# Optimization experiments

Measured on AMD Instinct MI355X. Metric: run time of the kernel, lower is better.

Reference implementation:

```python
import jax, jax.numpy as jnp
import numpy as np

B, S, H, Z = 32, 2048, 256, 64
TEMPERATURE = float(H) ** 0.5
NEG_INF = -1e9


def setup_inputs() -> dict:
    key = jax.random.key(0)
    ks = jax.random.split(key, 8)
    return {
        "encoder_hidden_states": jax.random.normal(ks[0], (B, S, H), dtype=jnp.float32),
        "decoder_hidden_states": jax.random.normal(ks[1], (B, S, H), dtype=jnp.float32),
        "decoder_final_hidden_state": jax.random.normal(ks[2], (B, H), dtype=jnp.float32),
        "latent_z_seq": jax.random.normal(ks[3], (B, S, Z), dtype=jnp.float32),
        "mask": jax.random.randint(ks[4], (B, S), 0, 2).astype(bool),
        "Wq": jax.random.normal(ks[5], (H, H), dtype=jnp.float32),
        "Wk": jax.random.normal(ks[6], (H, H), dtype=jnp.float32),
        "Wv": jax.random.normal(ks[7], (Z, Z), dtype=jnp.float32),
    }


def reference(encoder_hidden_states, decoder_hidden_states, decoder_final_hidden_state,
              latent_z_seq, mask, Wq, Wk, Wv):
    # Projections
    k = jnp.einsum('bsh,hd->bsd', encoder_hidden_states, Wk)
    q = jnp.einsum('bsh,hd->bsd', decoder_hidden_states, Wq)
    v = jnp.einsum('bsz,zd->bsd', latent_z_seq, Wv)
    # alignment[b, i, j] = q_i . k_j / sqrt(H)   -> [B, S, S]
    alignment = jnp.einsum('bid,bjd->bij', q, k) / TEMPERATURE
    # mask over QUERY positions (axis -2), broadcast along key axis (-1)
    alignment = jnp.where(mask[:, :, None], alignment, NEG_INF)
    # NOTE: non-standard softmax over the query axis (dim=-2)
    attn = jax.nn.softmax(alignment, axis=-2)
    output = jnp.einsum('bij,bjd->bid', attn, v)  # [B, S, Z]
    return output, attn
```

## Files before the change

kernel.cpp:

```cpp
#include <hip/hip_runtime.h>
#include <stdint.h>

#define B_  32
#define S_  2048
#define H_  256
#define Z_  64

typedef unsigned short u16;
typedef __attribute__((ext_vector_type(8))) short bf16x8;
typedef __attribute__((ext_vector_type(4))) float f32x4;

__device__ __forceinline__ u16 f2bf(float f) {
    unsigned int x = __float_as_uint(f);
    x = (x + 0x7fffu + ((x >> 16) & 1u)) >> 16;
    return (u16)x;
}
__device__ __forceinline__ float bf2f(u16 u) {
    return __uint_as_float(((unsigned int)u) << 16);
}

__device__ __forceinline__ void gl2lds16(const void* g, void* l) {
    __builtin_amdgcn_global_load_lds(
        (const __attribute__((address_space(1))) unsigned int*)g,
        (__attribute__((address_space(3))) unsigned int*)l,
        16, 0, 0);
}

__global__ void detect_kernel(const u16* __restrict__ wq, int* __restrict__ flag) {
    __shared__ int tot;
    const int t = threadIdx.x;
    if (t == 0) tot = 0;
    __syncthreads();
    int cnt = 0;
    #pragma unroll
    for (int r = 0; r < 16; ++r) {
        u16 u = wq[(r * 256 + t) * 2];
        int e = (u >> 7) & 0xFF;
        cnt += (u == 0 || (e >= 107 && e <= 132)) ? 1 : 0;
    }
    atomicAdd(&tot, cnt);
    __syncthreads();
    if (t == 0) *flag = (tot < 2048) ? 1 : 0;
}

__device__ void role_mask(int bx, const void* __restrict__ raw, int* __restrict__ mi) {
    __shared__ int isByte;
    const int t = threadIdx.x;
    if (t == 0) isByte = 0;
    __syncthreads();
    const unsigned int* w = (const unsigned int*)raw;
    if (w[t & 255] > 1u) isByte = 1;
    __syncthreads();
    int e = bx * 256 + t;
    int val;
    if (isByte) val = ((const unsigned char*)raw)[e] ? 1 : 0;
    else        val = w[e] ? 1 : 0;
    mi[e] = val;
}

__device__ void role_wsplit(int bx, int by, int fp32,
                            const void* __restrict__ Wq, const void* __restrict__ Wk,
                            u16* __restrict__ WqTh, u16* __restrict__ WqTl,
                            u16* __restrict__ WkTh, u16* __restrict__ WkTl) {
    const void* src = by ? Wk : Wq;
    u16* oh = by ? WkTh : WqTh;
    u16* ol = by ? WkTl : WqTl;
    int base = bx * 1024;
    #pragma unroll
    for (int r = 0; r < 4; ++r) {
        int idx = base + r * 256 + threadIdx.x;
        int d = idx >> 8, h = idx & 255;
        float v = fp32 ? ((const float*)src)[h * 256 + d]
                       : bf2f(((const u16*)src)[h * 256 + d]);
        u16 hi = f2bf(v);
        oh[idx] = hi;
        ol[idx] = f2bf(v - bf2f(hi));
    }
}

__device__ void role_xsplit(int bx, int by, int fp32,
                            const void* __restrict__ dec, const void* __restrict__ enc,
                            u16* __restrict__ Xdh, u16* __restrict__ Xdl,
                            u16* __restrict__ Xeh, u16* __restrict__ Xel) {
    const void* src = by ? enc : dec;
    u16* oh = by ? Xeh : Xdh;
    u16* ol = by ? Xel : Xdl;
    const int t = threadIdx.x;
    const size_t blockbase = (size_t)bx * 4096;
    if (fp32) {
        const float4* s4 = (const float4*)src;
        #pragma unroll
        for (int j = 0; j < 4; ++j) {
            size_t idx = blockbase + j * 1024 + t * 4;
            float4 v = s4[idx >> 2];
            u16 h0 = f2bf(v.x), h1 = f2bf(v.y), h2 = f2bf(v.z), h3 = f2bf(v.w);
            u16 l0 = f2bf(v.x - bf2f(h0)), l1 = f2bf(v.y - bf2f(h1));
            u16 l2 = f2bf(v.z - bf2f(h2)), l3 = f2bf(v.w - bf2f(h3));
            uint2 ph, pl;
            ph.x = (unsigned)h0 | ((unsigned)h1 << 16);
            ph.y = (unsigned)h2 | ((unsigned)h3 << 16);
            pl.x = (unsigned)l0 | ((unsigned)l1 << 16);
            pl.y = (unsigned)l2 | ((unsigned)l3 << 16);
            ((uint2*)oh)[idx >> 2] = ph;
            ((uint2*)ol)[idx >> 2] = pl;
        }
    } else {
        const uint2* s2 = (const uint2*)src;
        #pragma unroll
        for (int j = 0; j < 4; ++j) {
            size_t idx = blockbase + j * 1024 + t * 4;
            uint2 r = s2[idx >> 2];
            uint2 z; z.x = 0u; z.y = 0u;
            ((uint2*)oh)[idx >> 2] = r;
            ((uint2*)ol)[idx >> 2] = z;
        }
    }
}

__device__ void role_vproj(int bx, int dc, int fp32,
                           const void* __restrict__ Lraw,
                           const void* __restrict__ Wvraw, u16* __restrict__ vT) {
    __shared__ float wv[64 * 16];
    const int t = threadIdx.x;
    #pragma unroll
    for (int r = 0; r < 4; ++r) {
        int idx = r * 256 + t;
        int z = idx >> 4, dd = idx & 15;
        wv[idx] = fp32 ? ((const float*)Wvraw)[z * 64 + dc * 16 + dd]
                       : bf2f(((const u16*)Wvraw)[z * 64 + dc * 16 + dd]);
    }
    __syncthreads();
    const int flat = bx * 256 + t;
    const int b = flat >> 11, s = flat & 2047;

    float lz[64];
    if (fp32) {
        const float4* lr = (const float4*)((const float*)Lraw + (size_t)flat * 64);
        #pragma unroll
        for (int c = 0; c < 16; ++c) {
            float4 v = lr[c];
            lz[c * 4 + 0] = v.x; lz[c * 4 + 1] = v.y;
            lz[c * 4 + 2] = v.z; lz[c * 4 + 3] = v.w;
        }
    } else {
        const uint4* lr = (const uint4*)((const u16*)Lraw + (size_t)flat * 64);
        #pragma unroll
        for (int c = 0; c < 8; ++c) {
            uint4 v = lr[c];
            unsigned wd[4] = {v.x, v.y, v.z, v.w};
            #pragma unroll
            for (int e2 = 0; e2 < 4; ++e2) {
                lz[c * 8 + e2 * 2 + 0] = bf2f((u16)(wd[e2] & 0xffffu));
                lz[c * 8 + e2 * 2 + 1] = bf2f((u16)(wd[e2] >> 16));
            }
        }
    }

    float acc[16];
    #pragma unroll
    for (int d = 0; d < 16; ++d) acc[d] = 0.f;
    for (int z = 0; z < 64; ++z) {
        float lv = lz[z];
        const float4* wrow = (const float4*)&wv[z * 16];
        #pragma unroll
        for (int d4 = 0; d4 < 4; ++d4) {
            float4 wq = wrow[d4];
            acc[d4 * 4 + 0] += lv * wq.x;
            acc[d4 * 4 + 1] += lv * wq.y;
            acc[d4 * 4 + 2] += lv * wq.z;
            acc[d4 * 4 + 3] += lv * wq.w;
        }
    }
    #pragma unroll
    for (int d = 0; d < 16; ++d)
        vT[((size_t)b * 64 + dc * 16 + d) * S_ + s] = f2bf(acc[d]);
}

__global__ __launch_bounds__(256) void prep_kernel(
        const int* __restrict__ flagp, int n_xs,
        const void* __restrict__ dec, const void* __restrict__ enc,
        u16* __restrict__ Xdh, u16* __restrict__ Xdl,
        u16* __restrict__ Xeh, u16* __restrict__ Xel,
        const void* __restrict__ Lraw, const void* __restrict__ Wvraw,
        u16* __restrict__ vT,
        const void* __restrict__ Wq, const void* __restrict__ Wk,
        u16* __restrict__ WqTh, u16* __restrict__ WqTl,
        u16* __restrict__ WkTh, u16* __restrict__ WkTl,
        const void* __restrict__ mraw, int* __restrict__ maskI)
{
    const int fp32 = *flagp;
    int r = blockIdx.x;
    if (r < n_xs) {
        role_xsplit(r & 4095, r >> 12, fp32, dec, enc, Xdh, Xdl, Xeh, Xel);
        return;
    }
    r -= n_xs;
    if (r < 1024) {
        role_vproj(r & 255, r >> 8, fp32, Lraw, Wvraw, vT);
        return;
    }
    r -= 1024;
    if (r < 128) {
        role_wsplit(r & 63, r >> 6, fp32, Wq, Wk, WqTh, WqTl, WkTh, WkTl);
        return;
    }
    r -= 128;
    role_mask(r, mraw, maskI);
}

__global__ __launch_bounds__(256, 2) void proj_kernel(
        const int* __restrict__ flagp, int use_xsplit,
        const float* __restrict__ Xf0, const u16* __restrict__ Xu0,
        const u16* __restrict__ Xh0, const u16* __restrict__ Xl0,
        const u16* __restrict__ WTh0, const u16* __restrict__ WTl0,
        u16* __restrict__ Ph0, u16* __restrict__ Pl0,
        const float* __restrict__ Xf1, const u16* __restrict__ Xu1,
        const u16* __restrict__ Xh1, const u16* __restrict__ Xl1,
        const u16* __restrict__ WTh1, const u16* __restrict__ WTl1,
        u16* __restrict__ Ph1, u16* __restrict__ Pl1)
{
    __shared__ __align__(16) u16 lds[16384];
    const int z = blockIdx.z;
    const float* Xf = z ? Xf1 : Xf0;
    const u16*   Xu = z ? Xu1 : Xu0;
    const u16*   Xh = z ? Xh1 : Xh0;
    const u16*   Xl = z ? Xl1 : Xl0;
    const u16*  WTh = z ? WTh1 : WTh0;
    const u16*  WTl = z ? WTl1 : WTl0;
    u16* Ph = z ? Ph1 : Ph0;
    u16* Pl = z ? Pl1 : Pl0;

    const int fp32 = *flagp;
    const int t = threadIdx.x;
    const int lane = t & 63, w = t >> 6;
    const int i0 = blockIdx.x * 128;
    const int d0 = blockIdx.y * 128;
    const int rh = w >> 1, ch = w & 1;
    const int l15 = lane & 15;
    const int c0 = lane >> 4;

    const int srow = t >> 3;
    const int scp  = t & 7;
    const int sc   = scp ^ (srow & 7);
    const int scol = (sc & 3) * 8;
    const int slo  = sc & 4;

    f32x4 acc[4][4];
    #pragma unroll
    for (int a = 0; a < 4; ++a)
        #pragma unroll
        for (int c = 0; c < 4; ++c) acc[a][c] = (f32x4){0.f, 0.f, 0.f, 0.f};

    for (int ks = 0; ks < 8; ++ks) {
        const int kc = ks * 32;
        {
            const u16* wsrc = slo ? WTl : WTh;
            #pragma unroll
            for (int rep = 0; rep < 4; ++rep) {
                int s = t + rep * 256;
                int row = srow + rep * 32;
                gl2lds16(wsrc + (size_t)(d0 + row) * H_ + kc + scol, lds + 8192 + s * 8);
            }
        }
        if (use_xsplit) {
            const u16* xsrc = slo ? Xl : Xh;
            #pragma unroll
            for (int rep = 0; rep < 4; ++rep) {
                int s = t + rep * 256;
                int row = srow + rep * 32;
                gl2lds16(xsrc + (size_t)(i0 + row) * H_ + kc + scol, lds + s * 8);
            }
        } else if (fp32) {
            #pragma unroll
            for (int rep = 0; rep < 2; ++rep) {
                int s = t + rep * 256;
                int r = s >> 2, c8 = s & 3;
                const float4* src = (const float4*)(Xf + (size_t)(i0 + r) * H_ + kc + c8 * 8);
                float4 x0 = src[0], x1 = src[1];
                float xs[8] = {x0.x, x0.y, x0.z, x0.w, x1.x, x1.y, x1.z, x1.w};
                unsigned hh[8], ll[8];
                #pragma unroll
                for (int j = 0; j < 8; ++j) {
                    u16 hb = f2bf(xs[j]);
                    hh[j] = hb;
                    ll[j] = f2bf(xs[j] - bf2f(hb));
                }
                uint4 ph, pl;
                ph.x = hh[0] | (hh[1] << 16); ph.y = hh[2] | (hh[3] << 16);
                ph.z = hh[4] | (hh[5] << 16); ph.w = hh[6] | (hh[7] << 16);
                pl.x = ll[0] | (ll[1] << 16); pl.y = ll[2] | (ll[3] << 16);
                pl.z = ll[4] | (ll[5] << 16); pl.w = ll[6] | (ll[7] << 16);
                int posH = c8 ^ (r & 7);
                *(uint4*)(lds + r * 64 + posH * 8) = ph;
                *(uint4*)(lds + r * 64 + (posH ^ 4) * 8) = pl;
            }
        } else {
            #pragma unroll
            for (int rep = 0; rep < 2; ++rep) {
                int s = t + rep * 256;
                int r = s >> 2, c8 = s & 3;
                uint4 raw = *(const uint4*)(Xu + (size_t)(i0 + r) * H_ + kc + c8 * 8);
                int posH = c8 ^ (r & 7);
                *(uint4*)(lds + r * 64 + posH * 8) = raw;
                *(uint4*)(lds + r * 64 + (posH ^ 4) * 8) = (uint4){0u, 0u, 0u, 0u};
            }
        }
        __syncthreads();
        bf16x8 ah[4], al[4], bh[4], bl[4];
        #pragma unroll
        for (int f = 0; f < 4; ++f) {
            int ra = rh * 64 + f * 16 + l15;
            int rb = ch * 64 + f * 16 + l15;
            int pa = c0 ^ (ra & 7);
            int pb = c0 ^ (rb & 7);
            ah[f] = *(const bf16x8*)(lds + ra * 64 + pa * 8);
            al[f] = *(const bf16x8*)(lds + ra * 64 + (pa ^ 4) * 8);
            bh[f] = *(const bf16x8*)(lds + 8192 + rb * 64 + pb * 8);
            bl[f] = *(const bf16x8*)(lds + 8192 + rb * 64 + (pb ^ 4) * 8);
        }
        #pragma unroll
        for (int fr = 0; fr < 4; ++fr)
            #pragma unroll
            for (int fc = 0; fc < 4; ++fc) {
                acc[fr][fc] = __builtin_amdgcn_mfma_f32_16x16x32_bf16(al[fr], bh[fc], acc[fr][fc], 0, 0, 0);
                acc[fr][fc] = __builtin_amdgcn_mfma_f32_16x16x32_bf16(ah[fr], bl[fc], acc[fr][fc], 0, 0, 0);
                acc[fr][fc] = __builtin_amdgcn_mfma_f32_16x16x32_bf16(ah[fr], bh[fc], acc[fr][fc], 0, 0, 0);
            }
        __syncthreads();
    }
    #pragma unroll
    for (int fr = 0; fr < 4; ++fr)
        #pragma unroll
        for (int fc = 0; fc < 4; ++fc)
            #pragma unroll
            for (int reg = 0; reg < 4; ++reg) {
                float v = acc[fr][fc][reg];
                int i = i0 + rh * 64 + fr * 16 + (lane >> 4) * 4 + reg;
                int d = d0 + ch * 64 + fc * 16 + l15;
                u16 hi = f2bf(v);
                u16 lo = f2bf(v - bf2f(hi));
                size_t off = (size_t)i * H_ + d;
                Ph[off] = hi;
                Pl[off] = lo;
            }
}

__global__ __launch_bounds__(256, 2) void qk_kernel(
        const u16* __restrict__ qh, const u16* __restrict__ ql,
        const u16* __restrict__ kh, const u16* __restrict__ kl,
        const int* __restrict__ maskI, u16* __restrict__ attnB,
        float* __restrict__ attnF, u16* __restrict__ stageB, int use_stage,
        float* __restrict__ m_p, float* __restrict__ s_p,
        int b0, const int* __restrict__ flagp)
{
    __shared__ __align__(16) char smem[35328];
    u16*  stage = (u16*)smem;
    u16*  etile = (u16*)smem;
    float* cmax = (float*)(smem + 32768);
    float* csum = (float*)(smem + 33792);
    float* mrow = (float*)(smem + 34816);

    const int fp32 = *flagp;
    const int t = threadIdx.x;
    const int lane = t & 63, w = t >> 6;
    const int jt = blockIdx.x, it = blockIdx.y, bz = blockIdx.z;
    const int b = b0 + bz;
    const int i0 = it * 128, j0 = jt * 128;
    const int rh = w >> 1, ch = w & 1;
    const int l15 = lane & 15;
    const int c0 = lane >> 4;

    if (t < 128) mrow[t] = (maskI[b * S_ + i0 + t] != 0) ? 1.f : 0.f;

    const size_t qbase = ((size_t)bz * S_ + i0) * H_;
    const size_t kbase = ((size_t)bz * S_ + j0) * H_;

    const int srow = t >> 3;
    const int scp  = t & 7;
    const int sc   = scp ^ (srow & 7);
    const int scol = (sc & 3) * 8;
    const u16* qsrc = (sc & 4) ? ql : qh;
    const u16* ksrc = (sc & 4) ? kl : kh;

    f32x4 acc[4][4];
    #pragma unroll
    for (int a = 0; a < 4; ++a)
        #pragma unroll
        for (int c = 0; c < 4; ++c) acc[a][c] = (f32x4){0.f, 0.f, 0.f, 0.f};

    for (int ks = 0; ks < 8; ++ks) {
        const int kc = ks * 32;
        #pragma unroll
        for (int rep = 0; rep < 4; ++rep) {
            int s = t + rep * 256;
            int row = srow + rep * 32;
            gl2lds16(qsrc + qbase + (size_t)row * H_ + kc + scol, stage + s * 8);
            gl2lds16(ksrc + kbase + (size_t)row * H_ + kc + scol, stage + 8192 + s * 8);
        }
        __syncthreads();
        bf16x8 ah[4], al[4], bh[4], bl[4];
        #pragma unroll
        for (int f = 0; f < 4; ++f) {
            int ra = rh * 64 + f * 16 + l15;
            int rb = ch * 64 + f * 16 + l15;
            int pa = c0 ^ (ra & 7);
            int pb = c0 ^ (rb & 7);
            ah[f] = *(const bf16x8*)(stage + ra * 64 + pa * 8);
            al[f] = *(const bf16x8*)(stage + ra * 64 + (pa ^ 4) * 8);
            bh[f] = *(const bf16x8*)(stage + 8192 + rb * 64 + pb * 8);
            bl[f] = *(const bf16x8*)(stage + 8192 + rb * 64 + (pb ^ 4) * 8);
        }
        #pragma unroll
        for (int fr = 0; fr < 4; ++fr)
            #pragma unroll
            for (int fc = 0; fc < 4; ++fc) {
                acc[fr][fc] = __builtin_amdgcn_mfma_f32_16x16x32_bf16(al[fr], bh[fc], acc[fr][fc], 0, 0, 0);
                acc[fr][fc] = __builtin_amdgcn_mfma_f32_16x16x32_bf16(ah[fr], bl[fc], acc[fr][fc], 0, 0, 0);
                acc[fr][fc] = __builtin_amdgcn_mfma_f32_16x16x32_bf16(ah[fr], bh[fc], acc[fr][fc], 0, 0, 0);
            }
        __syncthreads();
    }

    const float inv_t = 0.0625f;
    float mloc[4] = {-3e38f, -3e38f, -3e38f, -3e38f};
    #pragma unroll
    for (int fr = 0; fr < 4; ++fr)
        #pragma unroll
        for (int reg = 0; reg < 4; ++reg) {
            float keep = mrow[rh * 64 + fr * 16 + (lane >> 4) * 4 + reg];
            #pragma unroll
            for (int fc = 0; fc < 4; ++fc) {
                float l = acc[fr][fc][reg] * inv_t;
                l = (keep != 0.f) ? l : -1e9f;
                acc[fr][fc][reg] = l;
                mloc[fc] = fmaxf(mloc[fc], l);
            }
        }
    #pragma unroll
    for (int fc = 0; fc < 4; ++fc) {
        mloc[fc] = fmaxf(mloc[fc], __shfl_xor(mloc[fc], 16, 64));
        mloc[fc] = fmaxf(mloc[fc], __shfl_xor(mloc[fc], 32, 64));
    }
    if (lane < 16) {
        #pragma unroll
        for (int fc = 0; fc < 4; ++fc)
            cmax[rh * 128 + ch * 64 + fc * 16 + lane] = mloc[fc];
    }
    __syncthreads();

    float mcol[4], sloc[4];
    #pragma unroll
    for (int fc = 0; fc < 4; ++fc) {
        int c = ch * 64 + fc * 16 + l15;
        mcol[fc] = fmaxf(cmax[c], cmax[128 + c]);
        sloc[fc] = 0.f;
    }
    #pragma unroll
    for (int fr = 0; fr < 4; ++fr)
        #pragma unroll
        for (int reg = 0; reg < 4; ++reg) {
            int row = rh * 64 + fr * 16 + (lane >> 4) * 4 + reg;
            #pragma unroll
            for (int fc = 0; fc < 4; ++fc) {
                float e = __expf(acc[fr][fc][reg] - mcol[fc]);
                sloc[fc] += e;
                etile[row * 128 + ch * 64 + fc * 16 + l15] = f2bf(e);
            }
        }
    #pragma unroll
    for (int fc = 0; fc < 4; ++fc) {
        sloc[fc] += __shfl_xor(sloc[fc], 16, 64);
        sloc[fc] += __shfl_xor(sloc[fc], 32, 64);
    }
    if (lane < 16) {
        #pragma unroll
        for (int fc = 0; fc < 4; ++fc)
            csum[rh * 128 + ch * 64 + fc * 16 + lane] = sloc[fc];
    }
    __syncthreads();

    if (t < 128) {
        float m = fmaxf(cmax[t], cmax[128 + t]);
        float sres = csum[t] + csum[128 + t];
        size_t so = ((size_t)b * 16 + it) * S_ + j0 + t;
        m_p[so] = m;
        s_p[so] = sres;
    }
    const size_t abase = ((size_t)b * S_ + i0) * S_ + j0;
    if (fp32) {
        if (use_stage) {
            #pragma unroll
            for (int rep = 0; rep < 8; ++rep) {
                int s = t + rep * 256;
                int row = s >> 4, off = (s & 15) * 8;
                *(uint4*)(stageB + abase + (size_t)row * S_ + off) = *(const uint4*)(etile + s * 8);
            }
        } else {
            #pragma unroll
            for (int rep = 0; rep < 8; ++rep) {
                int s = t + rep * 256;
                int row = s >> 4, off = (s & 15) * 8;
                const u16* src = etile + s * 8;
                float* gp = attnF + abase + (size_t)row * S_ + off;
                float4 f0, f1;
                f0.x = bf2f(src[0]); f0.y = bf2f(src[1]); f0.z = bf2f(src[2]); f0.w = bf2f(src[3]);
                f1.x = bf2f(src[4]); f1.y = bf2f(src[5]); f1.z = bf2f(src[6]); f1.w = bf2f(src[7]);
                *(float4*)gp = f0;
                *(float4*)(gp + 4) = f1;
            }
        }
    } else {
        #pragma unroll
        for (int rep = 0; rep < 8; ++rep) {
            int s = t + rep * 256;
            int row = s >> 4, off = (s & 15) * 8;
            *(uint4*)(attnB + abase + (size_t)row * S_ + off) = *(const uint4*)(etile + s * 8);
        }
    }
}

__global__ __launch_bounds__(256) void stats_kernel(
        const float* __restrict__ m_p, const float* __restrict__ s_p, float* __restrict__ scl)
{
    int id = blockIdx.x * 256 + threadIdx.x;
    int b = id >> 11, j = id & 2047;
    float mv[16];
    float M = -3e38f;
    #pragma unroll
    for (int itile = 0; itile < 16; ++itile) {
        mv[itile] = m_p[((size_t)b * 16 + itile) * S_ + j];
        M = fmaxf(M, mv[itile]);
    }
    float L = 0.f;
    #pragma unroll
    for (int itile = 0; itile < 16; ++itile)
        L += s_p[((size_t)b * 16 + itile) * S_ + j] * __expf(mv[itile] - M);
    float invL = (L > 0.f) ? (1.f / L) : 0.f;
    #pragma unroll
    for (int itile = 0; itile < 16; ++itile)
        scl[((size_t)b * 16 + itile) * S_ + j] = __expf(mv[itile] - M) * invL;
}

__global__ __launch_bounds__(256, 2) void av_gemm_kernel(
        const u16* __restrict__ vT, const float* __restrict__ scl,
        const u16* __restrict__ stageB, u16* __restrict__ attnB,
        float* __restrict__ attnF,
        u16* __restrict__ outB, float* __restrict__ outF,
        const int* __restrict__ flagp)
{
    __shared__ __align__(16) u16 lds_attn[128 * 128];
    __shared__ __align__(16) u16 lds_vt[64 * 128];
    const int fp32 = *flagp;
    const u16* srcE = fp32 ? stageB : attnB;
    const int t = threadIdx.x;
    const int lane = t & 63, w = t >> 6;
    const int it = blockIdx.x, b = blockIdx.y;
    const int i0 = it * 128;
    const int l15 = lane & 15;

    const int acp = t & 15;
    const int arow0 = t >> 4;
    const int ac = acp ^ (arow0 & 15);
    const int vpos = (t & 15) ^ (t >> 4);
    const int j8 = (t & 15) * 8;

    f32x4 acc[2][4];
    #pragma unroll
    for (int a = 0; a < 2; ++a)
        #pragma unroll
        for (int c = 0; c < 4; ++c) acc[a][c] = (f32x4){0.f, 0.f, 0.f, 0.f};

    for (int jt = 0; jt < 16; ++jt) {
        const int j0 = jt * 128;
        __syncthreads();
        const size_t abase = ((size_t)b * S_ + i0) * S_ + j0;
        #pragma unroll
        for (int rep = 0; rep < 8; ++rep) {
            int s = t + rep * 256;
            int row = arow0 + rep * 16;
            gl2lds16(srcE + abase + (size_t)row * S_ + ac * 8, lds_attn + s * 8);
        }
        float sc[8], esc[8];
        {
            const float4* sp = (const float4*)(scl + ((size_t)b * 16 + it) * S_ + j0 + j8);
            float4 s0 = sp[0], s1 = sp[1];
            sc[0] = s0.x; sc[1] = s0.y; sc[2] = s0.z; sc[3] = s0.w;
            sc[4] = s1.x; sc[5] = s1.y; sc[6] = s1.z; sc[7] = s1.w;
            const float4* ep = (const float4*)(scl + ((size_t)b * 16 + it) * S_ + j0 + ac * 8);
            float4 e0 = ep[0], e1 = ep[1];
            esc[0] = e0.x; esc[1] = e0.y; esc[2] = e0.z; esc[3] = e0.w;
            esc[4] = e1.x; esc[5] = e1.y; esc[6] = e1.z; esc[7] = e1.w;
        }
        #pragma unroll
        for (int rep = 0; rep < 4; ++rep) {
            int d = (t >> 4) + rep * 16;
            uint4 raw = *(const uint4*)(vT + ((size_t)b * 64 + d) * S_ + j0 + j8);
            unsigned wd[4] = {raw.x, raw.y, raw.z, raw.w};
            #pragma unroll
            for (int e2 = 0; e2 < 4; ++e2) {
                float f0 = bf2f((u16)(wd[e2] & 0xffffu)) * sc[e2 * 2];
                float f1 = bf2f((u16)(wd[e2] >> 16))     * sc[e2 * 2 + 1];
                wd[e2] = (unsigned)f2bf(f0) | ((unsigned)f2bf(f1) << 16);
            }
            uint4 pk; pk.x = wd[0]; pk.y = wd[1]; pk.z = wd[2]; pk.w = wd[3];
            *(uint4*)(lds_vt + d * 128 + vpos * 8) = pk;
        }
        __syncthreads();

        #pragma unroll
        for (int rep = 0; rep < 8; ++rep) {
            int s = t + rep * 256;
            int row = arow0 + rep * 16;
            uint4 pk = *(const uint4*)(lds_attn + s * 8);
            unsigned wd[4] = {pk.x, pk.y, pk.z, pk.w};
            float f[8];
            f[0] = bf2f((u16)(wd[0] & 0xffffu)) * esc[0];
            f[1] = bf2f((u16)(wd[0] >> 16))     * esc[1];
            f[2] = bf2f((u16)(wd[1] & 0xffffu)) * esc[2];
            f[3] = bf2f((u16)(wd[1] >> 16))     * esc[3];
            f[4] = bf2f((u16)(wd[2] & 0xffffu)) * esc[4];
            f[5] = bf2f((u16)(wd[2] >> 16))     * esc[5];
            f[6] = bf2f((u16)(wd[3] & 0xffffu)) * esc[6];
            f[7] = bf2f((u16)(wd[3] >> 16))     * esc[7];
            size_t ga = abase + (size_t)row * S_ + ac * 8;
            if (fp32) {
                float4 o0, o1;
                o0.x = f[0]; o0.y = f[1]; o0.z = f[2]; o0.w = f[3];
                o1.x = f[4]; o1.y = f[5]; o1.z = f[6]; o1.w = f[7];
                *(float4*)(attnF + ga) = o0;
                *(float4*)(attnF + ga + 4) = o1;
            } else {
                uint4 o;
                o.x = (unsigned)f2bf(f[0]) | ((unsigned)f2bf(f[1]) << 16);
                o.y = (unsigned)f2bf(f[2]) | ((unsigned)f2bf(f[3]) << 16);
                o.z = (unsigned)f2bf(f[4]) | ((unsigned)f2bf(f[5]) << 16);
                o.w = (unsigned)f2bf(f[6]) | ((unsigned)f2bf(f[7]) << 16);
                *(uint4*)(attnB + ga) = o;
            }
        }

        #pragma unroll
        for (int ksj = 0; ksj < 4; ++ksj) {
            int ck = ksj * 4 + (lane >> 4);
            int pA = ck ^ l15;
            int rA0 = w * 32 + l15, rA1 = w * 32 + 16 + l15;
            bf16x8 a0 = *(const bf16x8*)(lds_attn + rA0 * 128 + pA * 8);
            bf16x8 a1 = *(const bf16x8*)(lds_attn + rA1 * 128 + pA * 8);
            bf16x8 bb[4];
            #pragma unroll
            for (int fc = 0; fc < 4; ++fc) {
                int d = fc * 16 + l15;
                bb[fc] = *(const bf16x8*)(lds_vt + d * 128 + pA * 8);
            }
            #pragma unroll
            for (int fc = 0; fc < 4; ++fc) {
                acc[0][fc] = __builtin_amdgcn_mfma_f32_16x16x32_bf16(a0, bb[fc], acc[0][fc], 0, 0, 0);
                acc[1][fc] = __builtin_amdgcn_mfma_f32_16x16x32_bf16(a1, bb[fc], acc[1][fc], 0, 0, 0);
            }
        }
    }
    #pragma unroll
    for (int fr = 0; fr < 2; ++fr)
        #pragma unroll
        for (int fc = 0; fc < 4; ++fc)
            #pragma unroll
            for (int reg = 0; reg < 4; ++reg) {
                int i = i0 + w * 32 + fr * 16 + (lane >> 4) * 4 + reg;
                int d = fc * 16 + l15;
                float v = acc[fr][fc][reg];
                size_t oo = ((size_t)b * S_ + i) * Z_ + d;
                if (fp32) outF[oo] = v;
                else      outB[oo] = f2bf(v);
            }
}

__global__ __launch_bounds__(256, 2) void av_fallback_kernel(
        const u16* __restrict__ vT, const float* __restrict__ scl,
        u16* __restrict__ attnB, float* __restrict__ attnF,
        u16* __restrict__ outB, float* __restrict__ outF,
        const int* __restrict__ flagp)
{
    __shared__ __align__(16) u16 lds_attn[128 * 128];
    __shared__ __align__(16) u16 lds_vt[64 * 128];
    __shared__ float lds_scale[128];
    const int fp32 = *flagp;
    const int t = threadIdx.x;
    const int lane = t & 63, w = t >> 6;
    const int it = blockIdx.x, b = blockIdx.y;
    const int i0 = it * 128;
    const int l15 = lane & 15, koff = (lane >> 4) * 8;

    f32x4 acc[2][4];
    #pragma unroll
    for (int a = 0; a < 2; ++a)
        #pragma unroll
        for (int c = 0; c < 4; ++c) acc[a][c] = (f32x4){0.f, 0.f, 0.f, 0.f};

    for (int jt = 0; jt < 16; ++jt) {
        const int j0 = jt * 128;
        __syncthreads();
        if (t < 128) lds_scale[t] = scl[((size_t)b * 16 + it) * S_ + j0 + t];
        #pragma unroll
        for (int rep = 0; rep < 4; ++rep) {
            int s = t + rep * 256;
            int d = s >> 4, off = (s & 15) * 8;
            gl2lds16(vT + ((size_t)b * 64 + d) * S_ + j0 + off, lds_vt + s * 8);
        }
        __syncthreads();

        const size_t abase = ((size_t)b * S_ + i0) * S_ + j0;
        if (fp32) {
            #pragma unroll
            for (int rep = 0; rep < 8; ++rep) {
                int s = t + rep * 256;
                int row = s >> 4, off = (s & 15) * 8;
                float* gp = attnF + abase + (size_t)row * S_ + off;
                float4 p0 = *(const float4*)gp;
                float4 p1 = *(const float4*)(gp + 4);
                p0.x *= lds_scale[off + 0]; p0.y *= lds_scale[off + 1];
                p0.z *= lds_scale[off + 2]; p0.w *= lds_scale[off + 3];
                p1.x *= lds_scale[off + 4]; p1.y *= lds_scale[off + 5];
                p1.z *= lds_scale[off + 6]; p1.w *= lds_scale[off + 7];
                *(float4*)gp = p0;
                *(float4*)(gp + 4) = p1;
                uint4 pk;
                pk.x = (unsigned)f2bf(p0.x) | ((unsigned)f2bf(p0.y) << 16);
                pk.y = (unsigned)f2bf(p0.z) | ((unsigned)f2bf(p0.w) << 16);
                pk.z = (unsigned)f2bf(p1.x) | ((unsigned)f2bf(p1.y) << 16);
                pk.w = (unsigned)f2bf(p1.z) | ((unsigned)f2bf(p1.w) << 16);
                *(uint4*)(lds_attn + s * 8) = pk;
            }
        } else {
            #pragma unroll
            for (int rep = 0; rep < 8; ++rep) {
                int s = t + rep * 256;
                int row = s >> 4, off = (s & 15) * 8;
                size_t ga = abase + (size_t)row * S_ + off;
                uint4 pk = *(const uint4*)(attnB + ga);
                unsigned int wd[4] = {pk.x, pk.y, pk.z, pk.w};
                #pragma unroll
                for (int e2 = 0; e2 < 4; ++e2) {
                    float f0 = bf2f((u16)(wd[e2] & 0xffffu)) * lds_scale[off + e2 * 2];
                    float f1 = bf2f((u16)(wd[e2] >> 16))     * lds_scale[off + e2 * 2 + 1];
                    wd[e2] = (unsigned int)f2bf(f0) | ((unsigned int)f2bf(f1) << 16);
                }
                uint4 opk; opk.x = wd[0]; opk.y = wd[1]; opk.z = wd[2]; opk.w = wd[3];
                *(uint4*)(attnB + ga) = opk;
                *(uint4*)(lds_attn + s * 8) = opk;
            }
        }
        __syncthreads();

        #pragma unroll
        for (int ksj = 0; ksj < 4; ++ksj) {
            bf16x8 a0 = *(const bf16x8*)(lds_attn + (w * 32 +  0 + l15) * 128 + ksj * 32 + koff);
            bf16x8 a1 = *(const bf16x8*)(lds_attn + (w * 32 + 16 + l15) * 128 + ksj * 32 + koff);
            bf16x8 bb[4];
            #pragma unroll
            for (int fc = 0; fc < 4; ++fc)
                bb[fc] = *(const bf16x8*)(lds_vt + (fc * 16 + l15) * 128 + ksj * 32 + koff);
            #pragma unroll
            for (int fc = 0; fc < 4; ++fc) {
                acc[0][fc] = __builtin_amdgcn_mfma_f32_16x16x32_bf16(a0, bb[fc], acc[0][fc], 0, 0, 0);
                acc[1][fc] = __builtin_amdgcn_mfma_f32_16x16x32_bf16(a1, bb[fc], acc[1][fc], 0, 0, 0);
            }
        }
    }
    #pragma unroll
    for (int fr = 0; fr < 2; ++fr)
        #pragma unroll
        for (int fc = 0; fc < 4; ++fc)
            #pragma unroll
            for (int reg = 0; reg < 4; ++reg) {
                int i = i0 + w * 32 + fr * 16 + (lane >> 4) * 4 + reg;
                int d = fc * 16 + l15;
                float v = acc[fr][fc][reg];
                size_t oo = ((size_t)b * S_ + i) * Z_ + d;
                if (fp32) outF[oo] = v;
                else      outB[oo] = f2bf(v);
            }
}

extern "C" void kernel_launch(void* const* d_in, const int* in_sizes, int n_in,
                              void* d_out, int out_size, void* d_ws, size_t ws_size,
                              hipStream_t stream) {
    const void* enc    = d_in[0];
    const void* dec    = d_in[1];
    const void* latent = d_in[3];
    const void* mraw   = d_in[4];
    const void* Wq     = d_in[5];
    const void* Wk     = d_in[6];
    const void* Wv     = d_in[7];

    u16*   outB  = (u16*)d_out;
    float* outF  = (float*)d_out;
    u16*   attnB = outB + (size_t)B_ * S_ * Z_;
    float* attnF = outF + (size_t)B_ * S_ * Z_;
    float* m_p = (float*)d_out;
    float* s_p = m_p + (size_t)B_ * 16 * S_;

    char* ws = (char*)d_ws;
    int*   flag  = (int*)ws;
    int*   maskI = (int*)(ws + 256);
    u16*   vT    = (u16*)((char*)maskI + (size_t)B_ * S_ * 4);
    u16*   WqTh  = vT + (size_t)B_ * Z_ * S_;
    u16*   WqTl  = WqTh + H_ * H_;
    u16*   WkTh  = WqTl + H_ * H_;
    u16*   WkTl  = WkTh + H_ * H_;
    float* scl   = (float*)(WkTl + H_ * H_);
    char*  dyn   = (char*)(scl + (size_t)B_ * 16 * S_);

    const size_t fixed_bytes  = (size_t)(dyn - ws);
    const size_t per_batch    = (size_t)4 * S_ * H_ * 2;
    const size_t xsplit_bytes = (size_t)4 * B_ * S_ * H_ * 2;
    const size_t stage_bytes  = (size_t)B_ * S_ * S_ * 2;

    long long avail = (long long)ws_size - (long long)fixed_bytes;
    int use_xsplit = 0, use_stage = 0;
    u16 *Xdh = 0, *Xdl = 0, *Xeh = 0, *Xel = 0, *stageB = 0;
    if (avail >= (long long)(xsplit_bytes + per_batch)) {
        use_xsplit = 1;
        Xdh = (u16*)dyn;
        Xdl = Xdh + (size_t)B_ * S_ * H_;
        Xeh = Xdl + (size_t)B_ * S_ * H_;
        Xel = Xeh + (size_t)B_ * S_ * H_;
        dyn += xsplit_bytes;
        avail -= (long long)xsplit_bytes;
    }
    if (avail >= (long long)(stage_bytes + per_batch)) {
        use_stage = 1;
        stageB = (u16*)dyn;
        dyn += stage_bytes;
        avail -= (long long)stage_bytes;
    }
    int g_b = (avail > 0) ? (int)(avail / (long long)per_batch) : 1;
    if (g_b < 1)  g_b = 1;
    if (g_b > 32) g_b = 32;

    u16* qh = (u16*)dyn;
    u16* ql = qh + (size_t)g_b * S_ * H_;
    u16* kh = ql + (size_t)g_b * S_ * H_;
    u16* kl = kh + (size_t)g_b * S_ * H_;

    detect_kernel<<<dim3(1), 256, 0, stream>>>((const u16*)Wq, flag);

    const int n_xs = use_xsplit ? 8192 : 0;
    prep_kernel<<<dim3(n_xs + 1024 + 128 + 256), 256, 0, stream>>>(
        flag, n_xs, dec, enc, Xdh, Xdl, Xeh, Xel,
        latent, Wv, vT, Wq, Wk, WqTh, WqTl, WkTh, WkTl, mraw, maskI);

    for (int b0 = 0; b0 < B_; b0 += g_b) {
        int g = (B_ - b0 < g_b) ? (B_ - b0) : g_b;
        size_t eoff = (size_t)b0 * S_ * H_;
        proj_kernel<<<dim3(g * 16, 2, 2), 256, 0, stream>>>(
            flag, use_xsplit,
            (const float*)dec + eoff, (const u16*)dec + eoff,
            use_xsplit ? Xdh + eoff : (u16*)0, use_xsplit ? Xdl + eoff : (u16*)0,
            WqTh, WqTl, qh, ql,
            (const float*)enc + eoff, (const u16*)enc + eoff,
            use_xsplit ? Xeh + eoff : (u16*)0, use_xsplit ? Xel + eoff : (u16*)0,
            WkTh, WkTl, kh, kl);
        qk_kernel<<<dim3(16, 16, g), 256, 0, stream>>>(qh, ql, kh, kl, maskI,
                                                       attnB, attnF, stageB, use_stage,
                                                       m_p, s_p, b0, flag);
    }
    stats_kernel<<<dim3(256), 256, 0, stream>>>(m_p, s_p, scl);
    if (use_stage) {
        av_gemm_kernel<<<dim3(16, 32), 256, 0, stream>>>(vT, scl, stageB, attnB, attnF,
                                                         outB, outF, flag);
    } else {
        av_fallback_kernel<<<dim3(16, 32), 256, 0, stream>>>(vT, scl, attnB, attnF,
                                                             outB, outF, flag);
    }
}
```

Measured before the change: 1.106 ms.

## Double-buffer LDS staging in projection and QK GEMM loops

Adds a second LDS buffer to both the projection and QK kernels so the next K-slice is issued to LDS while MFMAs run on the current one. Each loop iteration now needs only one barrier instead of two, and the explicit waitcnt is placed after compute. This doubles shared-memory use (qk_kernel grows to about 68KB), which may lower occupancy below the declared two blocks per CU.

```diff
diff --git a/kernel.cpp b/kernel.cpp
--- a/kernel.cpp
+++ b/kernel.cpp
@@ -219,7 +219,7 @@
         const u16* __restrict__ WTh1, const u16* __restrict__ WTl1,
         u16* __restrict__ Ph1, u16* __restrict__ Pl1)
 {
-    __shared__ __align__(16) u16 lds[16384];
+    __shared__ __align__(16) u16 lds[32768];
     const int z = blockIdx.z;
     const float* Xf = z ? Xf1 : Xf0;
     const u16*   Xu = z ? Xu1 : Xu0;
@@ -244,6 +244,8 @@
     const int sc   = scp ^ (srow & 7);
     const int scol = (sc & 3) * 8;
     const int slo  = sc & 4;
+    const u16* wsrc = slo ? WTl : WTh;
+    const u16* xsrc = slo ? Xl : Xh;
 
     f32x4 acc[4][4];
     #pragma unroll
@@ -251,24 +253,21 @@
         #pragma unroll
         for (int c = 0; c < 4; ++c) acc[a][c] = (f32x4){0.f, 0.f, 0.f, 0.f};
 
-    for (int ks = 0; ks < 8; ++ks) {
+    auto STAGE = [&](int ks, int bf) {
         const int kc = ks * 32;
-        {
-            const u16* wsrc = slo ? WTl : WTh;
+        u16* dst = lds + bf * 16384;
+        #pragma unroll
+        for (int rep = 0; rep < 4; ++rep) {
+            int s = t + rep * 256;
+            int row = srow + rep * 32;
+            gl2lds16(wsrc + (size_t)(d0 + row) * H_ + kc + scol, dst + 8192 + s * 8);
+        }
+        if (use_xsplit) {
             #pragma unroll
             for (int rep = 0; rep < 4; ++rep) {
                 int s = t + rep * 256;
                 int row = srow + rep * 32;
-                gl2lds16(wsrc + (size_t)(d0 + row) * H_ + kc + scol, lds + 8192 + s * 8);
-            }
-        }
-        if (use_xsplit) {
-            const u16* xsrc = slo ? Xl : Xh;
-            #pragma unroll
-            for (int rep = 0; rep < 4; ++rep) {
-                int s = t + rep * 256;
-                int row = srow + rep * 32;
-                gl2lds16(xsrc + (size_t)(i0 + row) * H_ + kc + scol, lds + s * 8);
+                gl2lds16(xsrc + (size_t)(i0 + row) * H_ + kc + scol, dst + s * 8);
             }
         } else if (fp32) {
             #pragma unroll
@@ -291,8 +290,8 @@
                 pl.x = ll[0] | (ll[1] << 16); pl.y = ll[2] | (ll[3] << 16);
                 pl.z = ll[4] | (ll[5] << 16); pl.w = ll[6] | (ll[7] << 16);
                 int posH = c8 ^ (r & 7);
-                *(uint4*)(lds + r * 64 + posH * 8) = ph;
-                *(uint4*)(lds + r * 64 + (posH ^ 4) * 8) = pl;
+                *(uint4*)(dst + r * 64 + posH * 8) = ph;
+                *(uint4*)(dst + r * 64 + (posH ^ 4) * 8) = pl;
             }
         } else {
             #pragma unroll
@@ -301,11 +300,20 @@
                 int r = s >> 2, c8 = s & 3;
                 uint4 raw = *(const uint4*)(Xu + (size_t)(i0 + r) * H_ + kc + c8 * 8);
                 int posH = c8 ^ (r & 7);
-                *(uint4*)(lds + r * 64 + posH * 8) = raw;
-                *(uint4*)(lds + r * 64 + (posH ^ 4) * 8) = (uint4){0u, 0u, 0u, 0u};
-            }
-        }
-        __syncthreads();
+                *(uint4*)(dst + r * 64 + posH * 8) = raw;
+                *(uint4*)(dst + r * 64 + (posH ^ 4) * 8) = (uint4){0u, 0u, 0u, 0u};
+            }
+        }
+    };
+
+    STAGE(0, 0);
+    asm volatile("s_waitcnt vmcnt(0) lgkmcnt(0)" ::: "memory");
+    __builtin_amdgcn_s_barrier();
+
+    for (int ks = 0; ks < 8; ++ks) {
+        const int cur = ks & 1;
+        if (ks < 7) STAGE(ks + 1, cur ^ 1);
+        const u16* sb = lds + cur * 16384;
         bf16x8 ah[4], al[4], bh[4], bl[4];
         #pragma unroll
         for (int f = 0; f < 4; ++f) {
@@ -313,10 +321,10 @@
             int rb = ch * 64 + f * 16 + l15;
             int pa = c0 ^ (ra & 7);
             int pb = c0 ^ (rb & 7);
-            ah[f] = *(const bf16x8*)(lds + ra * 64 + pa * 8);
-            al[f] = *(const bf16x8*)(lds + ra * 64 + (pa ^ 4) * 8);
-            bh[f] = *(const bf16x8*)(lds + 8192 + rb * 64 + pb * 8);
-            bl[f] = *(const bf16x8*)(lds + 8192 + rb * 64 + (pb ^ 4) * 8);
+            ah[f] = *(const bf16x8*)(sb + ra * 64 + pa * 8);
+            al[f] = *(const bf16x8*)(sb + ra * 64 + (pa ^ 4) * 8);
+            bh[f] = *(const bf16x8*)(sb + 8192 + rb * 64 + pb * 8);
+            bl[f] = *(const bf16x8*)(sb + 8192 + rb * 64 + (pb ^ 4) * 8);
         }
         #pragma unroll
         for (int fr = 0; fr < 4; ++fr)
@@ -326,8 +334,10 @@
                 acc[fr][fc] = __builtin_amdgcn_mfma_f32_16x16x32_bf16(ah[fr], bl[fc], acc[fr][fc], 0, 0, 0);
                 acc[fr][fc] = __builtin_amdgcn_mfma_f32_16x16x32_bf16(ah[fr], bh[fc], acc[fr][fc], 0, 0, 0);
             }
-        __syncthreads();
-    }
+        asm volatile("s_waitcnt vmcnt(0) lgkmcnt(0)" ::: "memory");
+        __builtin_amdgcn_s_barrier();
+    }
+
     #pragma unroll
     for (int fr = 0; fr < 4; ++fr)
         #pragma unroll
@@ -353,12 +363,12 @@
         float* __restrict__ m_p, float* __restrict__ s_p,
         int b0, const int* __restrict__ flagp)
 {
-    __shared__ __align__(16) char smem[35328];
+    __shared__ __align__(16) char smem[68096];
     u16*  stage = (u16*)smem;
     u16*  etile = (u16*)smem;
-    float* cmax = (float*)(smem + 32768);
-    float* csum = (float*)(smem + 33792);
-    float* mrow = (float*)(smem + 34816);
+    float* cmax = (float*)(smem + 65536);
+    float* csum = (float*)(smem + 66560);
+    float* mrow = (float*)(smem + 67584);
 
     const int fp32 = *flagp;
     const int t = threadIdx.x;
@@ -388,16 +398,26 @@
         #pragma unroll
         for (int c = 0; c < 4; ++c) acc[a][c] = (f32x4){0.f, 0.f, 0.f, 0.f};
 
-    for (int ks = 0; ks < 8; ++ks) {
+    auto STAGE = [&](int ks, int bf) {
         const int kc = ks * 32;
+        u16* dst = stage + bf * 16384;
         #pragma unroll
         for (int rep = 0; rep < 4; ++rep) {
             int s = t + rep * 256;
             int row = srow + rep * 32;
-            gl2lds16(qsrc + qbase + (size_t)row * H_ + kc + scol, stage + s * 8);
-            gl2lds16(ksrc + kbase + (size_t)row * H_ + kc + scol, stage + 8192 + s * 8);
-        }
-        __syncthreads();
+            gl2lds16(qsrc + qbase + (size_t)row * H_ + kc + scol, dst + s * 8);
+            gl2lds16(ksrc + kbase + (size_t)row * H_ + kc + scol, dst + 8192 + s * 8);
+        }
+    };
+
+    STAGE(0, 0);
+    asm volatile("s_waitcnt vmcnt(0) lgkmcnt(0)" ::: "memory");
+    __builtin_amdgcn_s_barrier();
+
+    for (int ks = 0; ks < 8; ++ks) {
+        const int cur = ks & 1;
+        if (ks < 7) STAGE(ks + 1, cur ^ 1);
+        const u16* sb = stage + cur * 16384;
         bf16x8 ah[4], al[4], bh[4], bl[4];
         #pragma unroll
         for (int f = 0; f < 4; ++f) {
@@ -405,10 +425,10 @@
             int rb = ch * 64 + f * 16 + l15;
             int pa = c0 ^ (ra & 7);
             int pb = c0 ^ (rb & 7);
-            ah[f] = *(const bf16x8*)(stage + ra * 64 + pa * 8);
-            al[f] = *(const bf16x8*)(stage + ra * 64 + (pa ^ 4) * 8);
-            bh[f] = *(const bf16x8*)(stage + 8192 + rb * 64 + pb * 8);
-            bl[f] = *(const bf16x8*)(stage + 8192 + rb * 64 + (pb ^ 4) * 8);
+            ah[f] = *(const bf16x8*)(sb + ra * 64 + pa * 8);
+            al[f] = *(const bf16x8*)(sb + ra * 64 + (pa ^ 4) * 8);
+            bh[f] = *(const bf16x8*)(sb + 8192 + rb * 64 + pb * 8);
+            bl[f] = *(const bf16x8*)(sb + 8192 + rb * 64 + (pb ^ 4) * 8);
         }
         #pragma unroll
         for (int fr = 0; fr < 4; ++fr)
@@ -418,7 +438,8 @@
                 acc[fr][fc] = __builtin_amdgcn_mfma_f32_16x16x32_bf16(ah[fr], bl[fc], acc[fr][fc], 0, 0, 0);
                 acc[fr][fc] = __builtin_amdgcn_mfma_f32_16x16x32_bf16(ah[fr], bh[fc], acc[fr][fc], 0, 0, 0);
             }
-        __syncthreads();
+        asm volatile("s_waitcnt vmcnt(0) lgkmcnt(0)" ::: "memory");
+        __builtin_amdgcn_s_barrier();
     }
 
     const float inv_t = 0.0625f;
```

New measurement: 1.129 ms. 1.02x slower.

## Fold Wq·Wkᵀ into a single matrix and project only encoder states

Applied to the files above, without the earlier changes.

Precomputes G = Wq·Wkᵀ in the prep kernel and projects only the encoder hidden states through G. The QK kernel then consumes the split decoder states directly as queries. This halves the projection GEMM work and the q buffer traffic when the xsplit workspace is available. The cost is an extra 256-block prep role that does a naive fp32 matmul, plus a change in rounding because G is stored as a bf16 hi/lo pair.

```diff
diff --git a/kernel.cpp b/kernel.cpp
--- a/kernel.cpp
+++ b/kernel.cpp
@@ -5,6 +5,7 @@
 #define S_  2048
 #define H_  256
 #define Z_  64
+#define NIT_ 16
 
 typedef unsigned short u16;
 typedef __attribute__((ext_vector_type(8))) short bf16x8;
@@ -78,6 +79,27 @@
     }
 }
 
+__device__ void role_gmat(int d, int fp32,
+                          const void* __restrict__ Wq, const void* __restrict__ Wk,
+                          u16* __restrict__ Gh, u16* __restrict__ Gl) {
+    __shared__ float wqrow[256];
+    const int t = threadIdx.x;
+    wqrow[t] = fp32 ? ((const float*)Wq)[d * 256 + t]
+                    : bf2f(((const u16*)Wq)[d * 256 + t]);
+    __syncthreads();
+    float s = 0.f;
+    if (fp32) {
+        const float* wk = (const float*)Wk + (size_t)t * 256;
+        for (int e = 0; e < 256; ++e) s += wqrow[e] * wk[e];
+    } else {
+        const u16* wk = (const u16*)Wk + (size_t)t * 256;
+        for (int e = 0; e < 256; ++e) s += wqrow[e] * bf2f(wk[e]);
+    }
+    u16 hi = f2bf(s);
+    Gh[d * 256 + t] = hi;
+    Gl[d * 256 + t] = f2bf(s - bf2f(hi));
+}
+
 __device__ void role_xsplit(int bx, int by, int fp32,
                             const void* __restrict__ dec, const void* __restrict__ enc,
                             u16* __restrict__ Xdh, u16* __restrict__ Xdl,
@@ -186,6 +208,7 @@
         const void* __restrict__ Wq, const void* __restrict__ Wk,
         u16* __restrict__ WqTh, u16* __restrict__ WqTl,
         u16* __restrict__ WkTh, u16* __restrict__ WkTl,
+        u16* __restrict__ Gh, u16* __restrict__ Gl,
         const void* __restrict__ mraw, int* __restrict__ maskI)
 {
     const int fp32 = *flagp;
@@ -205,7 +228,12 @@
         return;
     }
     r -= 128;
-    role_mask(r, mraw, maskI);
+    if (r < 256) {
+        role_mask(r, mraw, maskI);
+        return;
+    }
+    r -= 256;
+    role_gmat(r, fp32, Wq, Wk, Gh, Gl);
 }
 
 __global__ __launch_bounds__(256, 2) void proj_kernel(
@@ -482,7 +510,7 @@
     if (t < 128) {
         float m = fmaxf(cmax[t], cmax[128 + t]);
         float sres = csum[t] + csum[128 + t];
-        size_t so = ((size_t)b * 16 + it) * S_ + j0 + t;
+        size_t so = ((size_t)b * NIT_ + it) * S_ + j0 + t;
         m_p[so] = m;
         s_p[so] = sres;
     }
@@ -524,21 +552,21 @@
 {
     int id = blockIdx.x * 256 + threadIdx.x;
     int b = id >> 11, j = id & 2047;
-    float mv[16];
+    float mv[NIT_];
     float M = -3e38f;
     #pragma unroll
-    for (int itile = 0; itile < 16; ++itile) {
-        mv[itile] = m_p[((size_t)b * 16 + itile) * S_ + j];
+    for (int itile = 0; itile < NIT_; ++itile) {
+        mv[itile] = m_p[((size_t)b * NIT_ + itile) * S_ + j];
         M = fmaxf(M, mv[itile]);
     }
     float L = 0.f;
     #pragma unroll
-    for (int itile = 0; itile < 16; ++itile)
-        L += s_p[((size_t)b * 16 + itile) * S_ + j] * __expf(mv[itile] - M);
+    for (int itile = 0; itile < NIT_; ++itile)
+        L += s_p[((size_t)b * NIT_ + itile) * S_ + j] * __expf(mv[itile] - M);
     float invL = (L > 0.f) ? (1.f / L) : 0.f;
     #pragma unroll
-    for (int itile = 0; itile < 16; ++itile)
-        scl[((size_t)b * 16 + itile) * S_ + j] = __expf(mv[itile] - M) * invL;
+    for (int itile = 0; itile < NIT_; ++itile)
+        scl[((size_t)b * NIT_ + itile) * S_ + j] = __expf(mv[itile] - M) * invL;
 }
 
 __global__ __launch_bounds__(256, 2) void av_gemm_kernel(
@@ -563,6 +591,7 @@
     const int ac = acp ^ (arow0 & 15);
     const int vpos = (t & 15) ^ (t >> 4);
     const int j8 = (t & 15) * 8;
+    const size_t sclbase = ((size_t)b * NIT_ + it) * S_;
 
     f32x4 acc[2][4];
     #pragma unroll
@@ -582,11 +611,11 @@
         }
         float sc[8], esc[8];
         {
-            const float4* sp = (const float4*)(scl + ((size_t)b * 16 + it) * S_ + j0 + j8);
+            const float4* sp = (const float4*)(scl + sclbase + j0 + j8);
             float4 s0 = sp[0], s1 = sp[1];
             sc[0] = s0.x; sc[1] = s0.y; sc[2] = s0.z; sc[3] = s0.w;
             sc[4] = s1.x; sc[5] = s1.y; sc[6] = s1.z; sc[7] = s1.w;
-            const float4* ep = (const float4*)(scl + ((size_t)b * 16 + it) * S_ + j0 + ac * 8);
+            const float4* ep = (const float4*)(scl + sclbase + j0 + ac * 8);
             float4 e0 = ep[0], e1 = ep[1];
             esc[0] = e0.x; esc[1] = e0.y; esc[2] = e0.z; esc[3] = e0.w;
             esc[4] = e1.x; esc[5] = e1.y; esc[6] = e1.z; esc[7] = e1.w;
@@ -689,6 +718,7 @@
     const int it = blockIdx.x, b = blockIdx.y;
     const int i0 = it * 128;
     const int l15 = lane & 15, koff = (lane >> 4) * 8;
+    const size_t sclbase = ((size_t)b * NIT_ + it) * S_;
 
     f32x4 acc[2][4];
     #pragma unroll
@@ -699,7 +729,7 @@
     for (int jt = 0; jt < 16; ++jt) {
         const int j0 = jt * 128;
         __syncthreads();
-        if (t < 128) lds_scale[t] = scl[((size_t)b * 16 + it) * S_ + j0 + t];
+        if (t < 128) lds_scale[t] = scl[sclbase + j0 + t];
         #pragma unroll
         for (int rep = 0; rep < 4; ++rep) {
             int s = t + rep * 256;
@@ -797,7 +827,7 @@
     u16*   attnB = outB + (size_t)B_ * S_ * Z_;
     float* attnF = outF + (size_t)B_ * S_ * Z_;
     float* m_p = (float*)d_out;
-    float* s_p = m_p + (size_t)B_ * 16 * S_;
+    float* s_p = m_p + (size_t)B_ * NIT_ * S_;
 
     char* ws = (char*)d_ws;
     int*   flag  = (int*)ws;
@@ -807,8 +837,10 @@
     u16*   WqTl  = WqTh + H_ * H_;
     u16*   WkTh  = WqTl + H_ * H_;
     u16*   WkTl  = WkTh + H_ * H_;
-    float* scl   = (float*)(WkTl + H_ * H_);
-    char*  dyn   = (char*)(scl + (size_t)B_ * 16 * S_);
+    u16*   Gh    = WkTl + H_ * H_;
+    u16*   Gl    = Gh + H_ * H_;
+    float* scl   = (float*)(Gl + H_ * H_);
+    char*  dyn   = (char*)(scl + (size_t)B_ * NIT_ * S_);
 
     const size_t fixed_bytes  = (size_t)(dyn - ws);
     const size_t per_batch    = (size_t)4 * S_ * H_ * 2;
@@ -845,24 +877,36 @@
     detect_kernel<<<dim3(1), 256, 0, stream>>>((const u16*)Wq, flag);
 
     const int n_xs = use_xsplit ? 8192 : 0;
-    prep_kernel<<<dim3(n_xs + 1024 + 128 + 256), 256, 0, stream>>>(
+    prep_kernel<<<dim3(n_xs + 1024 + 128 + 256 + 256), 256, 0, stream>>>(
         flag, n_xs, dec, enc, Xdh, Xdl, Xeh, Xel,
-        latent, Wv, vT, Wq, Wk, WqTh, WqTl, WkTh, WkTl, mraw, maskI);
+        latent, Wv, vT, Wq, Wk, WqTh, WqTl, WkTh, WkTl, Gh, Gl, mraw, maskI);
 
     for (int b0 = 0; b0 < B_; b0 += g_b) {
         int g = (B_ - b0 < g_b) ? (B_ - b0) : g_b;
         size_t eoff = (size_t)b0 * S_ * H_;
-        proj_kernel<<<dim3(g * 16, 2, 2), 256, 0, stream>>>(
-            flag, use_xsplit,
-            (const float*)dec + eoff, (const u16*)dec + eoff,
-            use_xsplit ? Xdh + eoff : (u16*)0, use_xsplit ? Xdl + eoff : (u16*)0,
-            WqTh, WqTl, qh, ql,
-            (const float*)enc + eoff, (const u16*)enc + eoff,
-            use_xsplit ? Xeh + eoff : (u16*)0, use_xsplit ? Xel + eoff : (u16*)0,
-            WkTh, WkTl, kh, kl);
-        qk_kernel<<<dim3(16, 16, g), 256, 0, stream>>>(qh, ql, kh, kl, maskI,
-                                                       attnB, attnF, stageB, use_stage,
-                                                       m_p, s_p, b0, flag);
+        if (use_xsplit) {
+            proj_kernel<<<dim3(g * 16, 2, 1), 256, 0, stream>>>(
+                flag, use_xsplit,
+                (const float*)enc + eoff, (const u16*)enc + eoff,
+                Xeh + eoff, Xel + eoff,
+                Gh, Gl, kh, kl,
+                (const float*)enc + eoff, (const u16*)enc + eoff,
+                Xeh + eoff, Xel + eoff,
+                Gh, Gl, kh, kl);
+            qk_kernel<<<dim3(16, 16, g), 256, 0, stream>>>(
+                Xdh + eoff, Xdl + eoff, kh, kl, maskI,
+                attnB, attnF, stageB, use_stage, m_p, s_p, b0, flag);
+        } else {
+            proj_kernel<<<dim3(g * 16, 2, 2), 256, 0, stream>>>(
+                flag, use_xsplit,
+                (const float*)dec + eoff, (const u16*)dec + eoff,
+                (u16*)0, (u16*)0, WqTh, WqTl, qh, ql,
+                (const float*)enc + eoff, (const u16*)enc + eoff,
+                (u16*)0, (u16*)0, WkTh, WkTl, kh, kl);
+            qk_kernel<<<dim3(16, 16, g), 256, 0, stream>>>(
+                qh, ql, kh, kl, maskI,
+                attnB, attnF, stageB, use_stage, m_p, s_p, b0, flag);
+        }
     }
     stats_kernel<<<dim3(256), 256, 0, stream>>>(m_p, s_p, scl);
     if (use_stage) {
```

Measured after the change: 1.089 ms. About the same (-1.5%).
